# Kernel tuning notes

Measured on AMD Instinct MI355X. Metric: run time of the kernel, lower is better.

## Reference

```python
import jax, jax.numpy as jnp
import numpy as np

# Junction-tree config: chain of NC cliques, each owning K new variables,
# parent separator = previous clique's K vars; S states per var; MLP hidden H.
B, NC, K, S, H = 512, 512, 4, 8, 128
D = 2 * K * S


def setup_inputs() -> dict:
    key = jax.random.key(0)
    ks = jax.random.split(key, 4)
    x = jax.random.randint(ks[0], (B, NC * K), 0, S, dtype=jnp.int32)
    sc = 0.05
    W1 = jax.random.normal(ks[1], (NC, D, H), jnp.float32) * sc
    b1 = jnp.zeros((NC, H), jnp.float32)
    W2 = jax.random.normal(ks[2], (NC, H, H), jnp.float32) * sc
    b2 = jnp.zeros((NC, H), jnp.float32)
    W3 = jax.random.normal(ks[3], (NC, H, S), jnp.float32) * sc
    b3 = jnp.zeros((NC, S), jnp.float32)
    return dict(x=x, W1=W1, b1=b1, W2=W2, b2=b2, W3=W3, b3=b3)


def reference(x, W1, b1, W2, b2, W3, b3):
    """fast_likelihood: per-clique log-prob [B, NC].

    Clique i owns vars [i*K,(i+1)*K); parent of clique i is clique i-1 (root=0
    conditions on a zero parent vector). Each clique runs a conditional
    autoregressive MLP over its K variables.
    """
    dtype = W1.dtype
    Bx = x.shape[0]
    xc = x.reshape(Bx, NC, K)                         # [B,NC,K] clique states
    oh = jax.nn.one_hot(xc, S, dtype=dtype)           # [B,NC,K,S]
    # Parent separator one-hot (root clique gets zeros) -> gather along tree.
    parent = jnp.concatenate([jnp.zeros_like(oh[:, :1]), oh[:, :-1]], axis=1)
    parent_flat = parent.reshape(Bx, NC, K * S)       # [B,NC,K*S]
    prefix_mask = (jnp.arange(K)[:, None] > jnp.arange(K)[None, :]).astype(dtype)  # [Kpos,Kvar]
    prefix = jnp.einsum('jk,bnks->bnjks', prefix_mask, oh).reshape(Bx, NC, K, K * S)
    inp = jnp.concatenate(
        [jnp.broadcast_to(parent_flat[:, :, None], prefix.shape), prefix], axis=-1
    )                                                 # [B,NC,K,D]
    h = jax.nn.relu(jnp.einsum('bnkd,ndh->bnkh', inp, W1) + b1[None, :, None])
    h = jax.nn.relu(jnp.einsum('bnkh,nhg->bnkg', h, W2) + b2[None, :, None])
    logits = jnp.einsum('bnkh,nhs->bnks', h, W3) + b3[None, :, None]
    logp = jax.nn.log_softmax(logits, axis=-1)        # [B,NC,K,S]
    logp_obs = jnp.take_along_axis(logp, xc[..., None], axis=-1)[..., 0]  # [B,NC,K]
    return logp_obs.sum(axis=-1)                      # [B,NC] per-clique logps
```

## Files before the change

kernel.cpp:

```cpp
#include <hip/hip_runtime.h>
#include <hip/hip_bf16.h>

typedef __bf16 bf16;
typedef __attribute__((ext_vector_type(4)))  __bf16 bf16x4;
typedef __attribute__((ext_vector_type(8)))  __bf16 bf16x8;
typedef __attribute__((ext_vector_type(16))) float  f32x16;

#define B_   512
#define NC_  512
#define K_   4
#define S_   8
#define H_   128
#define D_   64
#define XROW (NC_ * K_)
#define NITER 32

static __device__ __forceinline__ int swap23(int v) {
    return (v & ~12) | ((v & 4) << 1) | ((v & 8) >> 1);
}

__global__ __launch_bounds__(512, 4)
void jt_mlp_kernel(const int*   __restrict__ x,
                   const float* __restrict__ W1g, const float* __restrict__ b1g,
                   const float* __restrict__ W2g, const float* __restrict__ b2g,
                   const float* __restrict__ W3g, const float* __restrict__ b3g,
                   float* __restrict__ out)
{
    __shared__ __align__(16) bf16 SW2[128 * 128];
    __shared__ __align__(16) bf16 SWX[128 * 64];
    __shared__ __align__(16) bf16 SW3[8 * 128];
    __shared__ __align__(16) float LX[2][3][64][4];
    __shared__ __align__(16) bf16 OHLUT[16 * 8];

    const int tid  = threadIdx.x;
    const int lane = tid & 63;
    const int ws   = __builtin_amdgcn_readfirstlane(tid >> 6);
    const int g    = ws >> 2;
    const int qs   = ws & 3;
    const int l31  = lane & 31;
    const int lhi  = lane >> 5;
    const int kk   = l31 & 3;
    const int n    = blockIdx.x;

    const float* W1p = W1g + (size_t)n * (D_ * H_);
    const float* W2p = W2g + (size_t)n * (H_ * H_);
    const float* W3p = W3g + (size_t)n * (H_ * S_);
    const float* b1p = b1g + n * H_;
    const float* b2p = b2g + n * H_;
    const float* b3p = b3g + n * S_;

    const int p31 = swap23(l31);
    const bf16 one = (bf16)1.0f, zero = (bf16)0.0f;

    if (tid < 16) {
        bf16x8 v;
#pragma unroll
        for (int j = 0; j < 8; ++j) v[j] = (tid == j + 1) ? one : zero;
        *(bf16x8*)&OHLUT[tid * 8] = v;
    }
    if (tid < 256) {
        const int c0 = (tid & 31) * 4;
        const int k0 = (tid >> 5) * 8;
        float rows[8][4];
#pragma unroll
        for (int i = 0; i < 8; ++i) {
            float4 t4 = *(const float4*)(W1p + (k0 + i) * H_ + c0);
            if (n == 0 && k0 < 32) t4 = make_float4(0.f, 0.f, 0.f, 0.f);
            rows[i][0] = t4.x; rows[i][1] = t4.y; rows[i][2] = t4.z; rows[i][3] = t4.w;
        }
        if (k0 == 0) {
            const float4 bb = *(const float4*)(b1p + c0);
#pragma unroll
            for (int i = 0; i < 8; ++i) {
                rows[i][0] += bb.x; rows[i][1] += bb.y;
                rows[i][2] += bb.z; rows[i][3] += bb.w;
            }
        }
#pragma unroll
        for (int j2 = 0; j2 < 4; ++j2) {
            const int c = c0 + j2;
            const int p = (c & ~31) | swap23(c & 31);
            const int ch = (k0 >> 3) ^ (p & 7);
            bf16x4 lo, hi;
#pragma unroll
            for (int i = 0; i < 4; ++i) {
                lo[i] = (bf16)rows[i][j2];
                hi[i] = (bf16)rows[4 + i][j2];
            }
            *(bf16x4*)&SWX[p * 64 + ch * 8 + 0] = lo;
            *(bf16x4*)&SWX[p * 64 + ch * 8 + 4] = hi;
        }
    }
    {
        const int c0 = (tid & 31) * 4;
        const int k0 = (tid >> 5) * 8;
        float rows[8][4];
#pragma unroll
        for (int i = 0; i < 8; ++i) {
            const float4 t4 = *(const float4*)(W2p + (k0 + i) * H_ + c0);
            rows[i][0] = t4.x; rows[i][1] = t4.y; rows[i][2] = t4.z; rows[i][3] = t4.w;
        }
#pragma unroll
        for (int j2 = 0; j2 < 4; ++j2) {
            const int c = c0 + j2;
            const int p = (c & ~31) | swap23(c & 31);
            const int ch = (k0 >> 3) ^ (p & 15) ^ ((p & 16) >> 2);
            bf16x4 lo, hi;
#pragma unroll
            for (int i = 0; i < 4; ++i) {
                lo[i] = (bf16)rows[i][j2];
                hi[i] = (bf16)rows[4 + i][j2];
            }
            *(bf16x4*)&SW2[p * 128 + ch * 8 + 0] = lo;
            *(bf16x4*)&SW2[p * 128 + ch * 8 + 4] = hi;
        }
    }
    if (tid < 128) {
        const int s = tid >> 4, kc = tid & 15, k0 = kc * 8;
        float vv[8];
#pragma unroll
        for (int i = 0; i < 8; ++i) vv[i] = W3p[(k0 + i) * S_ + s];
        const int ch = kc ^ s;
        bf16x4 lo, hi;
#pragma unroll
        for (int i = 0; i < 4; ++i) { lo[i] = (bf16)vv[i]; hi[i] = (bf16)vv[4 + i]; }
        *(bf16x4*)&SW3[s * 128 + ch * 8 + 0] = lo;
        *(bf16x4*)&SW3[s * 128 + ch * 8 + 4] = hi;
    }
    __syncthreads();

    bf16x8 w1f[4];
#pragma unroll
    for (int kt = 0; kt < 4; ++kt)
        w1f[kt] = *(const bf16x8*)
            &SWX[(32 * qs + l31) * 64 + (((kt << 1) + lhi) ^ (l31 & 7)) * 8];
    const int s2 = l31 & 7;
    bf16x8 w3f[2];
#pragma unroll
    for (int e = 0; e < 2; ++e)
        w3f[e] = *(const bf16x8*)
            &SW3[s2 * 128 + ((((2 * qs + e) << 1) + lhi) ^ s2) * 8];
    bf16x8 w2b, onef;
#pragma unroll
    for (int j = 0; j < 8; ++j) { w2b[j] = zero; onef[j] = zero; }
    w2b[0] = lhi ? zero : (bf16)b2p[32 * qs + p31];
    onef[0] = lhi ? zero : one;
    const float4 b3q = *(const float4*)(b3p + 4 * lhi);

    f32x16 zf;
#pragma unroll
    for (int i = 0; i < 16; ++i) zf[i] = 0.f;

    __syncthreads();
    bf16* HX = SWX;

    const int itbase = g * 8 + (l31 >> 2);
    int4 xo_c, xp_c;
    {
        const int* xb = x + (size_t)itbase * XROW + n * K_;
        xo_c = *(const int4*)xb;
        xp_c = (n > 0) ? *(const int4*)(xb - K_) : make_int4(0, 0, 0, 0);
    }

    const int swz = (l31 & 15) ^ ((l31 & 16) >> 2);
    const int pq  = (32 * qs + l31) * 128;
    const int g8  = g * 8;

#pragma unroll 1
    for (int c = 0; c < NITER; ++c) {
        const int item = itbase + c * 16;
        const int4 xo = xo_c, xp = xp_c;
        if (c < NITER - 1) {
            const int* xb = x + (size_t)(item + 16) * XROW + n * K_;
            xo_c = *(const int4*)xb;
            xp_c = (n > 0) ? *(const int4*)(xb - K_) : make_int4(0, 0, 0, 0);
        }

        int sel[4];
        sel[0] = (n > 0) ? (lhi ? xp.y : xp.x) : (lhi ? -1 : 0);
        sel[1] = (n > 0) ? (lhi ? xp.w : xp.z) : -1;
        sel[2] = (kk > (lhi ? 1 : 0)) ? (lhi ? xo.y : xo.x) : -1;
        sel[3] = (kk > (lhi ? 3 : 2)) ? (lhi ? xo.w : xo.z) : -1;

        f32x16 A = zf;
#pragma unroll
        for (int kt = 0; kt < 4; ++kt) {
            const bf16x8 bf1 = *(const bf16x8*)&OHLUT[(sel[kt] + 1) * 8];
            A = __builtin_amdgcn_mfma_f32_32x32x16_bf16(w1f[kt], bf1, A, 0, 0, 0);
        }

#pragma unroll
        for (int e = 0; e < 2; ++e) {
            bf16x8 hf;
#pragma unroll
            for (int j = 0; j < 8; ++j)
                hf[j] = (bf16)fmaxf(A[8 * e + j], 0.f);
            *(bf16x8*)&HX[(g8 + 2 * qs + e) * 512 + lane * 8] = hf;
        }
        __syncthreads();

        f32x16 C = __builtin_amdgcn_mfma_f32_32x32x16_bf16(w2b, onef, zf, 0, 0, 0);
#pragma unroll
        for (int gc = 0; gc < 8; ++gc) {
            const bf16x8 hf = *(const bf16x8*)&HX[(g8 + gc) * 512 + lane * 8];
            const int chunk = ((gc << 1) + lhi) ^ swz;
            const bf16x8 f = *(const bf16x8*)&SW2[pq + chunk * 8];
            C = __builtin_amdgcn_mfma_f32_32x32x16_bf16(f, hf, C, 0, 0, 0);
        }

        f32x16 L = zf;
#pragma unroll
        for (int e = 0; e < 2; ++e) {
            bf16x8 hg;
#pragma unroll
            for (int j = 0; j < 8; ++j)
                hg[j] = (bf16)fmaxf(C[8 * e + j], 0.f);
            L = __builtin_amdgcn_mfma_f32_32x32x16_bf16(w3f[e], hg, L, 0, 0, 0);
        }

        if (qs != 0)
            *(float4*)&LX[g][qs - 1][lane][0] = make_float4(L[0], L[1], L[2], L[3]);
        __syncthreads();
        if (qs == 0) {
            const float4 P0 = *(const float4*)&LX[g][0][lane][0];
            const float4 P1 = *(const float4*)&LX[g][1][lane][0];
            const float4 P2 = *(const float4*)&LX[g][2][lane][0];
            float Ls0 = L[0] + P0.x + P1.x + P2.x + b3q.x;
            float Ls1 = L[1] + P0.y + P1.y + P2.y + b3q.y;
            float Ls2 = L[2] + P0.z + P1.z + P2.z + b3q.z;
            float Ls3 = L[3] + P0.w + P1.w + P2.w + b3q.w;

            float m4 = fmaxf(fmaxf(Ls0, Ls1), fmaxf(Ls2, Ls3));
            const float mm = fmaxf(m4, __shfl_xor(m4, 32));
            float e = __expf(Ls0 - mm) + __expf(Ls1 - mm) +
                      __expf(Ls2 - mm) + __expf(Ls3 - mm);
            const float ssum = e + __shfl_xor(e, 32);

            const int xs = (kk & 2) ? ((kk & 1) ? xo.w : xo.z)
                                    : ((kk & 1) ? xo.y : xo.x);
            const float own = (xs & 2) ? ((xs & 1) ? Ls3 : Ls2)
                                       : ((xs & 1) ? Ls1 : Ls0);
            const float oth = __shfl_xor(own, 32);
            const float obs = ((xs >> 2) == lhi) ? own : oth;
            float lp = obs - mm - __logf(ssum);
            lp += __shfl_xor(lp, 1);
            lp += __shfl_xor(lp, 2);
            if (lhi == 0 && kk == 0)
                out[(size_t)item * NC_ + n] = lp;
        }
    }
}

extern "C" void kernel_launch(void* const* d_in, const int* in_sizes, int n_in,
                              void* d_out, int out_size, void* d_ws, size_t ws_size,
                              hipStream_t stream) {
    const int*   x  = (const int*)d_in[0];
    const float* W1 = (const float*)d_in[1];
    const float* b1 = (const float*)d_in[2];
    const float* W2 = (const float*)d_in[3];
    const float* b2 = (const float*)d_in[4];
    const float* W3 = (const float*)d_in[5];
    const float* b3 = (const float*)d_in[6];
    float* out = (float*)d_out;
    jt_mlp_kernel<<<dim3(NC_), 512, 0, stream>>>(x, W1, b1, W2, b2, W3, b3, out);
}
```

Baseline: 165.1 us.

## Software-pipeline MLP layers with double-buffered hidden and logit buffers

Restructures the per-item loop so layer 1 for the next chunk runs in the same phase as layers 2–3 of the current chunk. The hidden activations and the partial logits are now double-buffered, which cuts the barriers per iteration from two to one. The softmax epilogue is deferred by one iteration. The barrier becomes a custom macro that waits only on LDS counters (lgkmcnt) before s_barrier. In exchange it uses more LDS, adds a prologue and epilogue peel, and needs more registers, which may hurt occupancy.

After: 156.5 us. -5.2%, faster.

```diff
diff --git a/kernel.cpp b/kernel.cpp
--- a/kernel.cpp
+++ b/kernel.cpp
@@ -19,6 +19,12 @@
     return (v & ~12) | ((v & 4) << 1) | ((v & 8) >> 1);
 }
 
+#define BARSYNC()                                            \
+    do {                                                     \
+        asm volatile("s_waitcnt lgkmcnt(0)" ::: "memory");   \
+        __builtin_amdgcn_s_barrier();                        \
+    } while (0)
+
 __global__ __launch_bounds__(512, 4)
 void jt_mlp_kernel(const int*   __restrict__ x,
                    const float* __restrict__ W1g, const float* __restrict__ b1g,
@@ -27,9 +33,10 @@
                    float* __restrict__ out)
 {
     __shared__ __align__(16) bf16 SW2[128 * 128];
-    __shared__ __align__(16) bf16 SWX[128 * 64];
+    __shared__ __align__(16) bf16 HX0[128 * 64];
+    __shared__ __align__(16) bf16 HX1[128 * 64];
     __shared__ __align__(16) bf16 SW3[8 * 128];
-    __shared__ __align__(16) float LX[2][3][64][4];
+    __shared__ __align__(16) float LX[2][2][3][64][4];
     __shared__ __align__(16) bf16 OHLUT[16 * 8];
 
     const int tid  = threadIdx.x;
@@ -87,8 +94,8 @@
                 lo[i] = (bf16)rows[i][j2];
                 hi[i] = (bf16)rows[4 + i][j2];
             }
-            *(bf16x4*)&SWX[p * 64 + ch * 8 + 0] = lo;
-            *(bf16x4*)&SWX[p * 64 + ch * 8 + 4] = hi;
+            *(bf16x4*)&HX0[p * 64 + ch * 8 + 0] = lo;
+            *(bf16x4*)&HX0[p * 64 + ch * 8 + 4] = hi;
         }
     }
     {
@@ -129,11 +136,15 @@
     }
     __syncthreads();
 
+    const int swz = (l31 & 15) ^ ((l31 & 16) >> 2);
+    const int pq  = (32 * qs + l31) * 128;
+    const int g8  = g * 8;
+
     bf16x8 w1f[4];
 #pragma unroll
     for (int kt = 0; kt < 4; ++kt)
         w1f[kt] = *(const bf16x8*)
-            &SWX[(32 * qs + l31) * 64 + (((kt << 1) + lhi) ^ (l31 & 7)) * 8];
+            &HX0[(32 * qs + l31) * 64 + (((kt << 1) + lhi) ^ (l31 & 7)) * 8];
     const int s2 = l31 & 7;
     bf16x8 w3f[2];
 #pragma unroll
@@ -151,63 +162,147 @@
 #pragma unroll
     for (int i = 0; i < 16; ++i) zf[i] = 0.f;
 
-    __syncthreads();
-    bf16* HX = SWX;
-
     const int itbase = g * 8 + (l31 >> 2);
-    int4 xo_c, xp_c;
+    int4 xo_c, xp_c, xo_e;
     {
         const int* xb = x + (size_t)itbase * XROW + n * K_;
         xo_c = *(const int4*)xb;
         xp_c = (n > 0) ? *(const int4*)(xb - K_) : make_int4(0, 0, 0, 0);
     }
 
-    const int swz = (l31 & 15) ^ ((l31 & 16) >> 2);
-    const int pq  = (32 * qs + l31) * 128;
-    const int g8  = g * 8;
-
-#pragma unroll 1
-    for (int c = 0; c < NITER; ++c) {
-        const int item = itbase + c * 16;
+    __syncthreads();
+
+    {
         const int4 xo = xo_c, xp = xp_c;
-        if (c < NITER - 1) {
-            const int* xb = x + (size_t)(item + 16) * XROW + n * K_;
+        {
+            const int* xb = x + (size_t)(itbase + 16) * XROW + n * K_;
             xo_c = *(const int4*)xb;
             xp_c = (n > 0) ? *(const int4*)(xb - K_) : make_int4(0, 0, 0, 0);
         }
-
         int sel[4];
         sel[0] = (n > 0) ? (lhi ? xp.y : xp.x) : (lhi ? -1 : 0);
         sel[1] = (n > 0) ? (lhi ? xp.w : xp.z) : -1;
         sel[2] = (kk > (lhi ? 1 : 0)) ? (lhi ? xo.y : xo.x) : -1;
         sel[3] = (kk > (lhi ? 3 : 2)) ? (lhi ? xo.w : xo.z) : -1;
-
         f32x16 A = zf;
 #pragma unroll
         for (int kt = 0; kt < 4; ++kt) {
             const bf16x8 bf1 = *(const bf16x8*)&OHLUT[(sel[kt] + 1) * 8];
             A = __builtin_amdgcn_mfma_f32_32x32x16_bf16(w1f[kt], bf1, A, 0, 0, 0);
         }
-
 #pragma unroll
         for (int e = 0; e < 2; ++e) {
             bf16x8 hf;
 #pragma unroll
             for (int j = 0; j < 8; ++j)
                 hf[j] = (bf16)fmaxf(A[8 * e + j], 0.f);
-            *(bf16x8*)&HX[(g8 + 2 * qs + e) * 512 + lane * 8] = hf;
-        }
-        __syncthreads();
-
-        f32x16 C = __builtin_amdgcn_mfma_f32_32x32x16_bf16(w2b, onef, zf, 0, 0, 0);
+            *(bf16x8*)&HX0[(g8 + 2 * qs + e) * 512 + lane * 8] = hf;
+        }
+        xo_e = xo;
+    }
+    BARSYNC();
+
+#define EPILOGUE(LXB, ITEME)                                                   \
+    if (qs == 0) {                                                             \
+        const float4 P0 = *(const float4*)&LX[LXB][g][0][lane][0];             \
+        const float4 P1 = *(const float4*)&LX[LXB][g][1][lane][0];             \
+        const float4 P2 = *(const float4*)&LX[LXB][g][2][lane][0];             \
+        float Ls0 = L[0] + P0.x + P1.x + P2.x + b3q.x;                         \
+        float Ls1 = L[1] + P0.y + P1.y + P2.y + b3q.y;                         \
+        float Ls2 = L[2] + P0.z + P1.z + P2.z + b3q.z;                         \
+        float Ls3 = L[3] + P0.w + P1.w + P2.w + b3q.w;                         \
+        float m4 = fmaxf(fmaxf(Ls0, Ls1), fmaxf(Ls2, Ls3));                    \
+        const float mm = fmaxf(m4, __shfl_xor(m4, 32));                        \
+        float ee = __expf(Ls0 - mm) + __expf(Ls1 - mm) +                       \
+                   __expf(Ls2 - mm) + __expf(Ls3 - mm);                        \
+        const float ssum = ee + __shfl_xor(ee, 32);                            \
+        const int xs = (kk & 2) ? ((kk & 1) ? xo_e.w : xo_e.z)                 \
+                                : ((kk & 1) ? xo_e.y : xo_e.x);                \
+        const float own = (xs & 2) ? ((xs & 1) ? Ls3 : Ls2)                    \
+                                   : ((xs & 1) ? Ls1 : Ls0);                   \
+        const float oth = __shfl_xor(own, 32);                                 \
+        const float obs = ((xs >> 2) == lhi) ? own : oth;                      \
+        float lp = obs - mm - __logf(ssum);                                    \
+        lp += __shfl_xor(lp, 1);                                               \
+        lp += __shfl_xor(lp, 2);                                               \
+        if (lhi == 0 && kk == 0)                                               \
+            out[(size_t)(ITEME) * NC_ + n] = lp;                               \
+    }
+
+#define ITER_BODY(KK, HR, HW, LXB)                                             \
+    do {                                                                       \
+        const int4 xo = xo_c, xp = xp_c;                                       \
+        if ((KK) < NITER - 1) {                                                \
+            const int* xb =                                                    \
+                x + (size_t)(itbase + ((KK) + 1) * 16) * XROW + n * K_;        \
+            xo_c = *(const int4*)xb;                                           \
+            xp_c = (n > 0) ? *(const int4*)(xb - K_) : make_int4(0, 0, 0, 0);  \
+        }                                                                      \
+                                        \
+        f32x16 C =                                                             \
+            __builtin_amdgcn_mfma_f32_32x32x16_bf16(w2b, onef, zf, 0, 0, 0);   \
+        _Pragma("unroll")                                                      \
+        for (int gc = 0; gc < 8; ++gc) {                                       \
+            const bf16x8 hf = *(const bf16x8*)&HR[(g8 + gc) * 512 + lane * 8]; \
+            const bf16x8 f =                                                   \
+                *(const bf16x8*)&SW2[pq + (((gc << 1) + lhi) ^ swz) * 8];      \
+            C = __builtin_amdgcn_mfma_f32_32x32x16_bf16(f, hf, C, 0, 0, 0);    \
+        }                                                                      \
+        f32x16 L = zf;                                                         \
+        _Pragma("unroll")                                                      \
+        for (int e = 0; e < 2; ++e) {                                          \
+            bf16x8 hg;                                                         \
+            _Pragma("unroll")                                                  \
+            for (int j = 0; j < 8; ++j)                                        \
+                hg[j] = (bf16)fmaxf(C[8 * e + j], 0.f);                        \
+            L = __builtin_amdgcn_mfma_f32_32x32x16_bf16(w3f[e], hg, L, 0, 0, 0);\
+        }                                                                      \
+        if (qs != 0)                                                           \
+            *(float4*)&LX[LXB][g][qs - 1][lane][0] =                           \
+                make_float4(L[0], L[1], L[2], L[3]);                           \
+                                            \
+        int sel[4];                                                            \
+        sel[0] = (n > 0) ? (lhi ? xp.y : xp.x) : (lhi ? -1 : 0);               \
+        sel[1] = (n > 0) ? (lhi ? xp.w : xp.z) : -1;                           \
+        sel[2] = (kk > (lhi ? 1 : 0)) ? (lhi ? xo.y : xo.x) : -1;              \
+        sel[3] = (kk > (lhi ? 3 : 2)) ? (lhi ? xo.w : xo.z) : -1;              \
+        f32x16 A = zf;                                                         \
+        _Pragma("unroll")                                                      \
+        for (int kt = 0; kt < 4; ++kt) {                                       \
+            const bf16x8 bf1 = *(const bf16x8*)&OHLUT[(sel[kt] + 1) * 8];      \
+            A = __builtin_amdgcn_mfma_f32_32x32x16_bf16(w1f[kt], bf1, A, 0, 0, 0);\
+        }                                                                      \
+        _Pragma("unroll")                                                      \
+        for (int e = 0; e < 2; ++e) {                                          \
+            bf16x8 hf;                                                         \
+            _Pragma("unroll")                                                  \
+            for (int j = 0; j < 8; ++j)                                        \
+                hf[j] = (bf16)fmaxf(A[8 * e + j], 0.f);                        \
+            *(bf16x8*)&HW[(g8 + 2 * qs + e) * 512 + lane * 8] = hf;            \
+        }                                                                      \
+        BARSYNC();                                                             \
+             \
+        EPILOGUE(LXB, itbase + ((KK) - 1) * 16)                                \
+        xo_e = xo;                                                             \
+    } while (0)
+
+#pragma unroll 1
+    for (int k = 1; k < NITER - 1; k += 2) {
+        ITER_BODY(k,     HX0, HX1, 0);
+        ITER_BODY(k + 1, HX1, HX0, 1);
+    }
+    ITER_BODY(NITER - 1, HX0, HX1, 0);
+
+    {
+        f32x16 C =
+            __builtin_amdgcn_mfma_f32_32x32x16_bf16(w2b, onef, zf, 0, 0, 0);
 #pragma unroll
         for (int gc = 0; gc < 8; ++gc) {
-            const bf16x8 hf = *(const bf16x8*)&HX[(g8 + gc) * 512 + lane * 8];
-            const int chunk = ((gc << 1) + lhi) ^ swz;
-            const bf16x8 f = *(const bf16x8*)&SW2[pq + chunk * 8];
+            const bf16x8 hf = *(const bf16x8*)&HX1[(g8 + gc) * 512 + lane * 8];
+            const bf16x8 f =
+                *(const bf16x8*)&SW2[pq + (((gc << 1) + lhi) ^ swz) * 8];
             C = __builtin_amdgcn_mfma_f32_32x32x16_bf16(f, hf, C, 0, 0, 0);
         }
-
         f32x16 L = zf;
 #pragma unroll
         for (int e = 0; e < 2; ++e) {
@@ -217,37 +312,11 @@
                 hg[j] = (bf16)fmaxf(C[8 * e + j], 0.f);
             L = __builtin_amdgcn_mfma_f32_32x32x16_bf16(w3f[e], hg, L, 0, 0, 0);
         }
-
         if (qs != 0)
-            *(float4*)&LX[g][qs - 1][lane][0] = make_float4(L[0], L[1], L[2], L[3]);
-        __syncthreads();
-        if (qs == 0) {
-            const float4 P0 = *(const float4*)&LX[g][0][lane][0];
-            const float4 P1 = *(const float4*)&LX[g][1][lane][0];
-            const float4 P2 = *(const float4*)&LX[g][2][lane][0];
-            float Ls0 = L[0] + P0.x + P1.x + P2.x + b3q.x;
-            float Ls1 = L[1] + P0.y + P1.y + P2.y + b3q.y;
-            float Ls2 = L[2] + P0.z + P1.z + P2.z + b3q.z;
-            float Ls3 = L[3] + P0.w + P1.w + P2.w + b3q.w;
-
-            float m4 = fmaxf(fmaxf(Ls0, Ls1), fmaxf(Ls2, Ls3));
-            const float mm = fmaxf(m4, __shfl_xor(m4, 32));
-            float e = __expf(Ls0 - mm) + __expf(Ls1 - mm) +
-                      __expf(Ls2 - mm) + __expf(Ls3 - mm);
-            const float ssum = e + __shfl_xor(e, 32);
-
-            const int xs = (kk & 2) ? ((kk & 1) ? xo.w : xo.z)
-                                    : ((kk & 1) ? xo.y : xo.x);
-            const float own = (xs & 2) ? ((xs & 1) ? Ls3 : Ls2)
-                                       : ((xs & 1) ? Ls1 : Ls0);
-            const float oth = __shfl_xor(own, 32);
-            const float obs = ((xs >> 2) == lhi) ? own : oth;
-            float lp = obs - mm - __logf(ssum);
-            lp += __shfl_xor(lp, 1);
-            lp += __shfl_xor(lp, 2);
-            if (lhi == 0 && kk == 0)
-                out[(size_t)item * NC_ + n] = lp;
-        }
+            *(float4*)&LX[1][g][qs - 1][lane][0] =
+                make_float4(L[0], L[1], L[2], L[3]);
+        BARSYNC();
+        EPILOGUE(1, itbase + (NITER - 1) * 16)
     }
 }
 
```
